# Kernel tuning notes

Measured on AMD Instinct MI355X. Metric: run time of the kernel, lower is better.

## Reference

```python
import jax, jax.numpy as jnp
import numpy as np

N, D_IN, H, L, K, Q = 131072, 384, 256, 32, 512, 4


def _lin_init(key, fan_in, fan_out):
    s = 1.0 / np.sqrt(fan_in)
    kw, kb = jax.random.split(key)
    w = jax.random.uniform(kw, (fan_in, fan_out), minval=-s, maxval=s, dtype=jnp.float32)
    b = jax.random.uniform(kb, (fan_out,), minval=-s, maxval=s, dtype=jnp.float32)
    return w, b


def setup_inputs() -> dict:
    key = jax.random.key(0)
    ks = jax.random.split(key, 8)
    enc_w1, enc_b1 = _lin_init(ks[1], D_IN, H)
    enc_w2, enc_b2 = _lin_init(ks[2], H, H)
    enc_w3, enc_b3 = _lin_init(ks[3], H, L)
    dec_w1, dec_b1 = _lin_init(ks[4], L, H)
    dec_w2, dec_b2 = _lin_init(ks[5], H, H)
    dec_w3, dec_b3 = _lin_init(ks[6], H, D_IN)
    codebooks = jax.random.normal(ks[7], (Q, K, L), dtype=jnp.float32) * 0.02
    x = jax.random.normal(ks[0], (N, D_IN), dtype=jnp.float32)
    return dict(x=x,
                enc_w1=enc_w1, enc_b1=enc_b1, enc_w2=enc_w2, enc_b2=enc_b2,
                enc_w3=enc_w3, enc_b3=enc_b3,
                dec_w1=dec_w1, dec_b1=dec_b1, dec_w2=dec_w2, dec_b2=dec_b2,
                dec_w3=dec_w3, dec_b3=dec_b3,
                codebooks=codebooks)


def _encoder(x, w1, b1, w2, b2, w3, b3):
    h = jax.nn.relu(x @ w1 + b1)
    h = jax.nn.relu(h @ w2 + b2)
    return h @ w3 + b3


def _decoder(z, w1, b1, w2, b2, w3, b3):
    h = jax.nn.relu(z @ w1 + b1)
    h = jax.nn.relu(h @ w2 + b2)
    return h @ w3 + b3


def _residual_vq(z, codebooks):
    """Residual VQ: Q stages of nearest-codeword lookup on the running residual.
    Returns (z_quantized with straight-through, indices [N,Q], commitment loss)."""
    residual = z
    quant_sum = jnp.zeros_like(z)
    indices = []
    commit = jnp.float32(0.0)
    for q in range(codebooks.shape[0]):  # small fixed loop over quantizer stages
        cb = codebooks[q]  # [K, L]
        # squared L2 distances [N, K] via expansion (cdist + argmin)
        d = (jnp.sum(residual * residual, axis=-1, keepdims=True)
             - 2.0 * residual @ cb.T
             + jnp.sum(cb * cb, axis=-1))
        idx = jnp.argmin(d, axis=-1)          # [N]
        qv = cb[idx]                          # gather [N, L]
        commit = commit + jnp.mean((jax.lax.stop_gradient(qv) - residual) ** 2)
        quant_sum = quant_sum + qv
        residual = residual - jax.lax.stop_gradient(qv)
        indices.append(idx)
    # straight-through estimator
    z_q = z + jax.lax.stop_gradient(quant_sum - z)
    return z_q, jnp.stack(indices, axis=-1), commit


def reference(x, enc_w1, enc_b1, enc_w2, enc_b2, enc_w3, enc_b3,
              dec_w1, dec_b1, dec_w2, dec_b2, dec_w3, dec_b3, codebooks):
    z = _encoder(x, enc_w1, enc_b1, enc_w2, enc_b2, enc_w3, enc_b3)
    z_q, indices, commit = _residual_vq(z, codebooks)
    x_recon = _decoder(z_q, dec_w1, dec_b1, dec_w2, dec_b2, dec_w3, dec_b3)
    return x_recon, indices, commit
```

## Files before the change

### kernel.cpp

```cpp
#include <hip/hip_runtime.h>
#include <hip/hip_bf16.h>
#include <math.h>


#define N_ROWS 131072
#define D_IN   384
#define H_DIM  256
#define L_DIM  32
#define K_CB   512
#define Q_ST   4
#define VQ_ROWS 256
#define NPART  (N_ROWS / VQ_ROWS)

typedef __attribute__((ext_vector_type(8))) short short8v;
typedef __attribute__((ext_vector_type(4))) float f32x4;

__device__ __forceinline__ ushort f2bf(float v)
{
    __hip_bfloat16 b = __float2bfloat16(v);
    return *reinterpret_cast<ushort*>(&b);
}

__device__ __forceinline__ float np_sumsq32(const float* __restrict__ v)
{
    #pragma clang fp contract(off)
    float s0 = v[0]*v[0], s1 = v[1]*v[1], s2 = v[2]*v[2], s3 = v[3]*v[3];
    float s4 = v[4]*v[4], s5 = v[5]*v[5], s6 = v[6]*v[6], s7 = v[7]*v[7];
    s0 = s0 + v[8]*v[8];   s1 = s1 + v[9]*v[9];   s2 = s2 + v[10]*v[10]; s3 = s3 + v[11]*v[11];
    s4 = s4 + v[12]*v[12]; s5 = s5 + v[13]*v[13]; s6 = s6 + v[14]*v[14]; s7 = s7 + v[15]*v[15];
    s0 = s0 + v[16]*v[16]; s1 = s1 + v[17]*v[17]; s2 = s2 + v[18]*v[18]; s3 = s3 + v[19]*v[19];
    s4 = s4 + v[20]*v[20]; s5 = s5 + v[21]*v[21]; s6 = s6 + v[22]*v[22]; s7 = s7 + v[23]*v[23];
    s0 = s0 + v[24]*v[24]; s1 = s1 + v[25]*v[25]; s2 = s2 + v[26]*v[26]; s3 = s3 + v[27]*v[27];
    s4 = s4 + v[28]*v[28]; s5 = s5 + v[29]*v[29]; s6 = s6 + v[30]*v[30]; s7 = s7 + v[31]*v[31];
    return ((s0 + s1) + (s2 + s3)) + ((s4 + s5) + (s6 + s7));
}

template<bool RELU>
__global__ __launch_bounds__(256)
void gemm_bias(const float* __restrict__ A, const float* __restrict__ B,
               const float* __restrict__ bias, float* __restrict__ C,
               int K, int Nout)
{
    #pragma clang fp contract(off)
    __shared__ float As2[32][132];
    __shared__ float Bs[32][128];
    const int t  = threadIdx.x;
    const int tc = t & 15;
    const int tr = t >> 4;
    const size_t row0 = (size_t)blockIdx.x * 128;
    const int    col0 = blockIdx.y * 128;

    float acc[8][8];
    #pragma unroll
    for (int i = 0; i < 8; ++i)
        #pragma unroll
        for (int j = 0; j < 8; ++j) acc[i][j] = 0.f;

    const int ar = t >> 3, ak = (t & 7) << 2;
    const int br = t >> 5, bc = (t & 31) << 2;

    for (int k0 = 0; k0 < K; k0 += 32) {
        #pragma unroll
        for (int i = 0; i < 4; ++i) {
            int r = ar + (i << 5);
            float4 v = *reinterpret_cast<const float4*>(A + (row0 + r) * (size_t)K + k0 + ak);
            As2[ak + 0][r] = v.x; As2[ak + 1][r] = v.y;
            As2[ak + 2][r] = v.z; As2[ak + 3][r] = v.w;
        }
        #pragma unroll
        for (int i = 0; i < 4; ++i) {
            int r = br + (i << 3);
            float4 v = *reinterpret_cast<const float4*>(B + (size_t)(k0 + r) * Nout + col0 + bc);
            *reinterpret_cast<float4*>(&Bs[r][bc]) = v;
        }
        __syncthreads();
        #pragma unroll
        for (int k = 0; k < 32; ++k) {
            float a[8], b[8];
            *reinterpret_cast<float4*>(&a[0]) = *reinterpret_cast<const float4*>(&As2[k][tr << 3]);
            *reinterpret_cast<float4*>(&a[4]) = *reinterpret_cast<const float4*>(&As2[k][(tr << 3) + 4]);
            *reinterpret_cast<float4*>(&b[0]) = *reinterpret_cast<const float4*>(&Bs[k][tc << 2]);
            *reinterpret_cast<float4*>(&b[4]) = *reinterpret_cast<const float4*>(&Bs[k][(tc << 2) + 64]);
            #pragma unroll
            for (int i = 0; i < 8; ++i)
                #pragma unroll
                for (int j = 0; j < 8; ++j) acc[i][j] = fmaf(a[i], b[j], acc[i][j]);
        }
        __syncthreads();
    }

    #pragma unroll
    for (int i = 0; i < 8; ++i) {
        size_t r = row0 + (tr << 3) + i;
        int c1 = col0 + (tc << 2);
        int c2 = c1 + 64;
        float v1[4], v2[4];
        #pragma unroll
        for (int j = 0; j < 4; ++j) {
            float u1 = acc[i][j]     + bias[c1 + j];
            float u2 = acc[i][j + 4] + bias[c2 + j];
            if (RELU) { u1 = fmaxf(u1, 0.0f); u2 = fmaxf(u2, 0.0f); }
            v1[j] = u1; v2[j] = u2;
        }
        *reinterpret_cast<float4*>(C + r * Nout + c1) = *reinterpret_cast<float4*>(&v1[0]);
        *reinterpret_cast<float4*>(C + r * Nout + c2) = *reinterpret_cast<float4*>(&v2[0]);
    }
}

__global__ __launch_bounds__(256)
void gemm_z(const float* __restrict__ A, const float* __restrict__ W,
            const float* __restrict__ bv, float* __restrict__ Z)
{
    #pragma clang fp contract(off)
    __shared__ float As2[32][132];
    __shared__ float Ws[32][36];
    const int t = threadIdx.x;
    const int cgz = t & 7, rgz = t >> 3;
    const size_t row0 = (size_t)blockIdx.x * 128;

    float acc[4][4];
    #pragma unroll
    for (int i = 0; i < 4; ++i)
        #pragma unroll
        for (int j = 0; j < 4; ++j) acc[i][j] = 0.f;

    const int ar = t >> 3, ak = (t & 7) << 2;
    for (int k0 = 0; k0 < H_DIM; k0 += 32) {
        #pragma unroll
        for (int i = 0; i < 4; ++i) {
            int r = ar + (i << 5);
            float4 v = *reinterpret_cast<const float4*>(A + (row0 + r) * (size_t)H_DIM + k0 + ak);
            As2[ak + 0][r] = v.x; As2[ak + 1][r] = v.y;
            As2[ak + 2][r] = v.z; As2[ak + 3][r] = v.w;
        }
        {
            int kr = t >> 3, cc = (t & 7) << 2;
            float4 v = *reinterpret_cast<const float4*>(W + (size_t)(k0 + kr) * L_DIM + cc);
            *reinterpret_cast<float4*>(&Ws[kr][cc]) = v;
        }
        __syncthreads();
        #pragma unroll
        for (int k = 0; k < 32; ++k) {
            float a[4], w[4];
            *reinterpret_cast<float4*>(&a[0]) = *reinterpret_cast<const float4*>(&As2[k][rgz << 2]);
            *reinterpret_cast<float4*>(&w[0]) = *reinterpret_cast<const float4*>(&Ws[k][cgz << 2]);
            #pragma unroll
            for (int i = 0; i < 4; ++i)
                #pragma unroll
                for (int j = 0; j < 4; ++j) acc[i][j] = fmaf(a[i], w[j], acc[i][j]);
        }
        __syncthreads();
    }
    #pragma unroll
    for (int i = 0; i < 4; ++i) {
        size_t row = row0 + (rgz << 2) + i;
        float v[4];
        #pragma unroll
        for (int j = 0; j < 4; ++j) v[j] = acc[i][j] + bv[(cgz << 2) + j];
        *reinterpret_cast<float4*>(Z + row * L_DIM + (cgz << 2)) = *reinterpret_cast<float4*>(&v[0]);
    }
}

__global__ __launch_bounds__(256)
void cnorm_kernel(const float* __restrict__ cbs, float* __restrict__ cnorm)
{
    #pragma clang fp contract(off)
    int g = blockIdx.x * 256 + threadIdx.x;
    const float* c = cbs + (size_t)g * L_DIM;
    float cl[L_DIM];
    #pragma unroll
    for (int l = 0; l < L_DIM; ++l) cl[l] = c[l];
    cnorm[g] = np_sumsq32(cl);
}

__global__ __launch_bounds__(256)
void prep_wt(const float* __restrict__ W, ushort* __restrict__ Wt, int K, int N)
{
    int g = blockIdx.x * 256 + threadIdx.x;
    if (g >= K * N) return;
    int n = g / K, k = g - n * K;
    Wt[g] = f2bf(W[(size_t)k * N + n]);
}

__global__ __launch_bounds__(256, 2)
void vq3_kernel(const float* __restrict__ zbuf, const float* __restrict__ cbs,
                const float* __restrict__ cnorm_g, ushort* __restrict__ zqb,
                float* __restrict__ idxOut, double* __restrict__ commitPart,
                int rowBase)
{
    #pragma clang fp contract(off)
    __shared__ float  cbL[K_CB * L_DIM];
    __shared__ float  cnL[K_CB];
    __shared__ double sred[256];

    const int t = threadIdx.x;
    const size_t lrow = (size_t)blockIdx.x * VQ_ROWS + t;
    const size_t grow = (size_t)rowBase + lrow;

    float z[L_DIM], r[L_DIM];
    {
        const float4* zp = reinterpret_cast<const float4*>(zbuf + lrow * L_DIM);
        #pragma unroll
        for (int j = 0; j < 8; ++j) {
            float4 v = zp[j];
            z[4*j+0]=v.x; z[4*j+1]=v.y; z[4*j+2]=v.z; z[4*j+3]=v.w;
        }
        #pragma unroll
        for (int l = 0; l < L_DIM; ++l) r[l] = z[l];
    }

    int bidx[Q_ST];
    double cAcc = 0.0;

    #pragma unroll 1
    for (int q = 0; q < Q_ST; ++q) {
        __syncthreads();
        {
            const float4* src = reinterpret_cast<const float4*>(cbs + (size_t)q * K_CB * L_DIM);
            float4* dst = reinterpret_cast<float4*>(cbL);
            #pragma unroll
            for (int i = 0; i < 16; ++i) dst[t + (i << 8)] = src[t + (i << 8)];
            cnL[t]       = cnorm_g[q * K_CB + t];
            cnL[t + 256] = cnorm_g[q * K_CB + t + 256];
        }
        __syncthreads();

        float rr = np_sumsq32(r);
        float bd = __builtin_inff();
        int   bi = 0;
        #pragma unroll 1
        for (int c = 0; c < K_CB; c += 2) {
            const float4* w0 = reinterpret_cast<const float4*>(cbL + (c << 5));
            const float4* w1 = w0 + 8;
            float a0 = 0.f, a1 = 0.f;
            #pragma unroll
            for (int j = 0; j < 8; ++j) {
                float4 u = w0[j], v = w1[j];
                a0 = fmaf(r[4*j+0], u.x, a0);  a1 = fmaf(r[4*j+0], v.x, a1);
                a0 = fmaf(r[4*j+1], u.y, a0);  a1 = fmaf(r[4*j+1], v.y, a1);
                a0 = fmaf(r[4*j+2], u.z, a0);  a1 = fmaf(r[4*j+2], v.z, a1);
                a0 = fmaf(r[4*j+3], u.w, a0);  a1 = fmaf(r[4*j+3], v.w, a1);
            }
            float d0 = (rr - 2.0f * a0) + cnL[c];
            float d1 = (rr - 2.0f * a1) + cnL[c + 1];
            if (d0 < bd) { bd = d0; bi = c; }
            if (d1 < bd) { bd = d1; bi = c + 1; }
        }
        bidx[q] = bi;

        {
            const float4* pw = reinterpret_cast<const float4*>(cbL + (bi << 5));
            float cs = 0.f;
            #pragma unroll
            for (int j = 0; j < 8; ++j) {
                float4 v = pw[j];
                float df;
                df = v.x - r[4*j+0]; cs = fmaf(df, df, cs); r[4*j+0] = r[4*j+0] - v.x;
                df = v.y - r[4*j+1]; cs = fmaf(df, df, cs); r[4*j+1] = r[4*j+1] - v.y;
                df = v.z - r[4*j+2]; cs = fmaf(df, df, cs); r[4*j+2] = r[4*j+2] - v.z;
                df = v.w - r[4*j+3]; cs = fmaf(df, df, cs); r[4*j+3] = r[4*j+3] - v.w;
            }
            cAcc += (double)cs;
        }
    }

    {
        float4 iv = make_float4((float)bidx[0], (float)bidx[1], (float)bidx[2], (float)bidx[3]);
        *reinterpret_cast<float4*>(idxOut + grow * Q_ST) = iv;
    }

    {
        ushort zq16[L_DIM];
        #pragma unroll
        for (int l = 0; l < L_DIM; ++l) zq16[l] = f2bf(z[l] - r[l]);
        uint4* o = reinterpret_cast<uint4*>(zqb + lrow * L_DIM);
        const uint4* s = reinterpret_cast<const uint4*>(zq16);
        #pragma unroll
        for (int j = 0; j < 4; ++j) o[j] = s[j];
    }

    sred[t] = cAcc;
    __syncthreads();
    for (int s = 128; s > 0; s >>= 1) {
        if (t < s) sred[t] += sred[t + s];
        __syncthreads();
    }
    if (t == 0) commitPart[rowBase / VQ_ROWS + blockIdx.x] = sred[0];
}

template<bool RELU, bool OUTBF16>
__global__ __launch_bounds__(256)
void mfma_gemm(const ushort* __restrict__ A, const ushort* __restrict__ Bt,
               const float* __restrict__ bias, void* __restrict__ Cout,
               int K, int Nout)
{
    __shared__ ushort As[128][40];
    __shared__ ushort Bs[128][40];
    const int t    = threadIdx.x;
    const int lane = t & 63;
    const int wid  = t >> 6;
    const int wr = wid >> 1, wc = wid & 1;
    const size_t row0 = (size_t)blockIdx.x * 128;
    const int    col0 = blockIdx.y * 128;

    f32x4 acc[4][4] = {};
    const int srow = t >> 1;
    const int sh   = (t & 1) << 4;

    for (int k0 = 0; k0 < K; k0 += 32) {
        {
            const ushort* ap = A + (row0 + srow) * (size_t)K + k0 + sh;
            uint4 v0 = *reinterpret_cast<const uint4*>(ap);
            uint4 v1 = *reinterpret_cast<const uint4*>(ap + 8);
            *reinterpret_cast<uint4*>(&As[srow][sh])     = v0;
            *reinterpret_cast<uint4*>(&As[srow][sh + 8]) = v1;
            const ushort* bp = Bt + (size_t)(col0 + srow) * K + k0 + sh;
            uint4 w0 = *reinterpret_cast<const uint4*>(bp);
            uint4 w1 = *reinterpret_cast<const uint4*>(bp + 8);
            *reinterpret_cast<uint4*>(&Bs[srow][sh])     = w0;
            *reinterpret_cast<uint4*>(&Bs[srow][sh + 8]) = w1;
        }
        __syncthreads();
        const int l15 = lane & 15, lk = (lane >> 4) << 3;
        short8v af[4], bf[4];
        #pragma unroll
        for (int f = 0; f < 4; ++f) {
            af[f] = *reinterpret_cast<const short8v*>(&As[(wr << 6) + (f << 4) + l15][lk]);
            bf[f] = *reinterpret_cast<const short8v*>(&Bs[(wc << 6) + (f << 4) + l15][lk]);
        }
        #pragma unroll
        for (int i = 0; i < 4; ++i)
            #pragma unroll
            for (int j = 0; j < 4; ++j)
                acc[i][j] = __builtin_amdgcn_mfma_f32_16x16x32_bf16(af[i], bf[j], acc[i][j], 0, 0, 0);
        __syncthreads();
    }

    const int l15 = lane & 15, lr4 = (lane >> 4) << 2;
    #pragma unroll
    for (int i = 0; i < 4; ++i) {
        #pragma unroll
        for (int j = 0; j < 4; ++j) {
            int col = col0 + (wc << 6) + (j << 4) + l15;
            float bv = bias[col];
            #pragma unroll
            for (int rj = 0; rj < 4; ++rj) {
                size_t row = row0 + (wr << 6) + (i << 4) + lr4 + rj;
                float v = acc[i][j][rj] + bv;
                if (RELU) v = fmaxf(v, 0.f);
                if (OUTBF16)
                    reinterpret_cast<ushort*>(Cout)[row * Nout + col] = f2bf(v);
                else
                    reinterpret_cast<float*>(Cout)[row * Nout + col] = v;
            }
        }
    }
}

__global__ __launch_bounds__(256)
void commit_finalize(const double* __restrict__ commitPart, float* __restrict__ outCommit)
{
    __shared__ double sred[256];
    const int t = threadIdx.x;
    double s = 0.0;
    for (int i = t; i < NPART; i += 256) s += commitPart[i];
    sred[t] = s;
    __syncthreads();
    for (int st = 128; st > 0; st >>= 1) {
        if (t < st) sred[t] += sred[t + st];
        __syncthreads();
    }
    if (t == 0)
        outCommit[0] = (float)(sred[0] / ((double)N_ROWS * (double)L_DIM));
}

extern "C" void kernel_launch(void* const* d_in, const int* in_sizes, int n_in,
                              void* d_out, int out_size, void* d_ws, size_t ws_size,
                              hipStream_t stream)
{
    const float* x      = (const float*)d_in[0];
    const float* enc_w1 = (const float*)d_in[1];
    const float* enc_b1 = (const float*)d_in[2];
    const float* enc_w2 = (const float*)d_in[3];
    const float* enc_b2 = (const float*)d_in[4];
    const float* enc_w3 = (const float*)d_in[5];
    const float* enc_b3 = (const float*)d_in[6];
    const float* dec_w1 = (const float*)d_in[7];
    const float* dec_b1 = (const float*)d_in[8];
    const float* dec_w2 = (const float*)d_in[9];
    const float* dec_b2 = (const float*)d_in[10];
    const float* dec_w3 = (const float*)d_in[11];
    const float* dec_b3 = (const float*)d_in[12];
    const float* cbs    = (const float*)d_in[13];

    float* out       = (float*)d_out;
    float* xrec      = out;
    float* idxOut    = out + (size_t)N_ROWS * D_IN;
    float* commitOut = idxOut + (size_t)N_ROWS * Q_ST;

    char*   wsb        = (char*)d_ws;
    float*  cnorm      = (float*)wsb;
    double* commitPart = (double*)(wsb + 8192);
    ushort* w1t        = (ushort*)(wsb + 12288);
    ushort* w2t        = (ushort*)(wsb + 28672);
    ushort* w3t        = (ushort*)(wsb + 159744);
    char*   bufs       = wsb + 360448;

    size_t availB = (ws_size > 360448) ? ws_size - 360448 : 0;
    long long chunk = (long long)(availB / 3264);
    chunk = (chunk / 256) * 256;
    if (chunk > N_ROWS) chunk = N_ROWS;
    if (chunk < 256) chunk = 256;

    float*  zbuf = (float*)bufs;
    float*  bufA = zbuf + (size_t)chunk * L_DIM;
    float*  bufB = bufA + (size_t)chunk * H_DIM;
    ushort* zqb  = (ushort*)(bufB + (size_t)chunk * H_DIM);
    ushort* h1b  = zqb + (size_t)chunk * L_DIM;
    ushort* h2b  = h1b + (size_t)chunk * H_DIM;

    cnorm_kernel<<<8, 256, 0, stream>>>(cbs, cnorm);
    prep_wt<<<(L_DIM  * H_DIM + 255) / 256, 256, 0, stream>>>(dec_w1, w1t, L_DIM, H_DIM);
    prep_wt<<<(H_DIM * H_DIM + 255) / 256, 256, 0, stream>>>(dec_w2, w2t, H_DIM, H_DIM);
    prep_wt<<<(H_DIM * D_IN + 255) / 256, 256, 0, stream>>>(dec_w3, w3t, H_DIM, D_IN);

    for (long long ro = 0; ro < N_ROWS; ro += chunk) {
        long long R = N_ROWS - ro;
        if (R > chunk) R = chunk;
        dim3 g2((unsigned)(R / 128), 2);
        dim3 g3((unsigned)(R / 128), 3);
        gemm_bias<true><<<g2, 256, 0, stream>>>(x + ro * D_IN, enc_w1, enc_b1, bufA, D_IN, H_DIM);
        gemm_bias<true><<<g2, 256, 0, stream>>>(bufA, enc_w2, enc_b2, bufB, H_DIM, H_DIM);
        gemm_z<<<(unsigned)(R / 128), 256, 0, stream>>>(bufB, enc_w3, enc_b3, zbuf);
        vq3_kernel<<<(unsigned)(R / VQ_ROWS), 256, 0, stream>>>(zbuf, cbs, cnorm, zqb,
                                                                idxOut, commitPart, (int)ro);
        mfma_gemm<true,  true ><<<g2, 256, 0, stream>>>(zqb, w1t, dec_b1, h1b, L_DIM, H_DIM);
        mfma_gemm<true,  true ><<<g2, 256, 0, stream>>>(h1b, w2t, dec_b2, h2b, H_DIM, H_DIM);
        mfma_gemm<false, false><<<g3, 256, 0, stream>>>(h2b, w3t, dec_b3, xrec + ro * D_IN, H_DIM, D_IN);
    }

    commit_finalize<<<1, 256, 0, stream>>>(commitPart, commitOut);
}
```

Baseline: 946.0 us.

## Split VQ codebook search across four waves per row and drop LDS staging

The VQ kernel now handles 64 rows per block, and each of the four waves scans a 128-entry slice of the codebook for the same rows. Per-wave minima are merged through shared memory, and codeword reads come straight from global memory instead of a shared-memory copy of the whole codebook. This removes the 64KB LDS footprint, raising occupancy and quadrupling the number of blocks available to fill the GPU. In exchange it adds two block syncs per stage and depends on cache-served, wave-uniform global loads. The commitPart buffer grows, so the workspace offsets move.

```diff
diff --git a/kernel.cpp b/kernel.cpp
--- a/kernel.cpp
+++ b/kernel.cpp
@@ -9,8 +9,8 @@
 #define L_DIM  32
 #define K_CB   512
 #define Q_ST   4
-#define VQ_ROWS 256
-#define NPART  (N_ROWS / VQ_ROWS)
+#define VQ_RPB 64
+#define NPART  (N_ROWS / VQ_RPB)
 
 typedef __attribute__((ext_vector_type(8))) short short8v;
 typedef __attribute__((ext_vector_type(4))) float f32x4;
@@ -182,31 +182,32 @@
     Wt[g] = f2bf(W[(size_t)k * N + n]);
 }
 
-__global__ __launch_bounds__(256, 2)
-void vq3_kernel(const float* __restrict__ zbuf, const float* __restrict__ cbs,
+__global__ __launch_bounds__(256)
+void vq6_kernel(const float* __restrict__ zbuf, const float* __restrict__ cbs,
                 const float* __restrict__ cnorm_g, ushort* __restrict__ zqb,
                 float* __restrict__ idxOut, double* __restrict__ commitPart,
                 int rowBase)
 {
     #pragma clang fp contract(off)
-    __shared__ float  cbL[K_CB * L_DIM];
-    __shared__ float  cnL[K_CB];
+    __shared__ float  sd[4][64];
+    __shared__ int    si[4][64];
     __shared__ double sred[256];
 
     const int t = threadIdx.x;
-    const size_t lrow = (size_t)blockIdx.x * VQ_ROWS + t;
+    const int w = t >> 6;
+    const int l = t & 63;
+    const size_t lrow = (size_t)blockIdx.x * VQ_RPB + l;
     const size_t grow = (size_t)rowBase + lrow;
-
-    float z[L_DIM], r[L_DIM];
+    const int c0 = w << 7;
+
+    float r[L_DIM];
     {
         const float4* zp = reinterpret_cast<const float4*>(zbuf + lrow * L_DIM);
         #pragma unroll
         for (int j = 0; j < 8; ++j) {
             float4 v = zp[j];
-            z[4*j+0]=v.x; z[4*j+1]=v.y; z[4*j+2]=v.z; z[4*j+3]=v.w;
-        }
-        #pragma unroll
-        for (int l = 0; l < L_DIM; ++l) r[l] = z[l];
+            r[4*j+0]=v.x; r[4*j+1]=v.y; r[4*j+2]=v.z; r[4*j+3]=v.w;
+        }
     }
 
     int bidx[Q_ST];
@@ -214,23 +215,17 @@
 
     #pragma unroll 1
     for (int q = 0; q < Q_ST; ++q) {
-        __syncthreads();
-        {
-            const float4* src = reinterpret_cast<const float4*>(cbs + (size_t)q * K_CB * L_DIM);
-            float4* dst = reinterpret_cast<float4*>(cbL);
-            #pragma unroll
-            for (int i = 0; i < 16; ++i) dst[t + (i << 8)] = src[t + (i << 8)];
-            cnL[t]       = cnorm_g[q * K_CB + t];
-            cnL[t + 256] = cnorm_g[q * K_CB + t + 256];
-        }
-        __syncthreads();
+        const float* cbq = cbs + (size_t)q * K_CB * L_DIM;
+        const float* cnq = cnorm_g + q * K_CB;
 
         float rr = np_sumsq32(r);
         float bd = __builtin_inff();
-        int   bi = 0;
-        #pragma unroll 1
-        for (int c = 0; c < K_CB; c += 2) {
-            const float4* w0 = reinterpret_cast<const float4*>(cbL + (c << 5));
+        int   bi = c0;
+
+        #pragma unroll 2
+        for (int cc = 0; cc < 128; cc += 2) {
+            const int c = c0 + cc;
+            const float4* w0 = reinterpret_cast<const float4*>(cbq + ((size_t)c << 5));
             const float4* w1 = w0 + 8;
             float a0 = 0.f, a1 = 0.f;
             #pragma unroll
@@ -241,15 +236,27 @@
                 a0 = fmaf(r[4*j+2], u.z, a0);  a1 = fmaf(r[4*j+2], v.z, a1);
                 a0 = fmaf(r[4*j+3], u.w, a0);  a1 = fmaf(r[4*j+3], v.w, a1);
             }
-            float d0 = (rr - 2.0f * a0) + cnL[c];
-            float d1 = (rr - 2.0f * a1) + cnL[c + 1];
+            float d0 = (rr - 2.0f * a0) + cnq[c];
+            float d1 = (rr - 2.0f * a1) + cnq[c + 1];
             if (d0 < bd) { bd = d0; bi = c; }
             if (d1 < bd) { bd = d1; bi = c + 1; }
         }
-        bidx[q] = bi;
+
+        __syncthreads();
+        sd[w][l] = bd;
+        si[w][l] = bi;
+        __syncthreads();
+
+        float gb = sd[0][l]; int gi = si[0][l];
+        #pragma unroll
+        for (int ww = 1; ww < 4; ++ww) {
+            float od = sd[ww][l]; int oi = si[ww][l];
+            if (od < gb) { gb = od; gi = oi; }
+        }
+        bidx[q] = gi;
 
         {
-            const float4* pw = reinterpret_cast<const float4*>(cbL + (bi << 5));
+            const float4* pw = reinterpret_cast<const float4*>(cbq + ((size_t)gi << 5));
             float cs = 0.f;
             #pragma unroll
             for (int j = 0; j < 8; ++j) {
@@ -264,28 +271,33 @@
         }
     }
 
-    {
+    if (w == 0) {
         float4 iv = make_float4((float)bidx[0], (float)bidx[1], (float)bidx[2], (float)bidx[3]);
         *reinterpret_cast<float4*>(idxOut + grow * Q_ST) = iv;
-    }
-
-    {
+
+        const float4* zp = reinterpret_cast<const float4*>(zbuf + lrow * L_DIM);
         ushort zq16[L_DIM];
         #pragma unroll
-        for (int l = 0; l < L_DIM; ++l) zq16[l] = f2bf(z[l] - r[l]);
+        for (int j = 0; j < 8; ++j) {
+            float4 v = zp[j];
+            zq16[4*j+0] = f2bf(v.x - r[4*j+0]);
+            zq16[4*j+1] = f2bf(v.y - r[4*j+1]);
+            zq16[4*j+2] = f2bf(v.z - r[4*j+2]);
+            zq16[4*j+3] = f2bf(v.w - r[4*j+3]);
+        }
         uint4* o = reinterpret_cast<uint4*>(zqb + lrow * L_DIM);
         const uint4* s = reinterpret_cast<const uint4*>(zq16);
         #pragma unroll
         for (int j = 0; j < 4; ++j) o[j] = s[j];
     }
 
-    sred[t] = cAcc;
+    sred[t] = (w == 0) ? cAcc : 0.0;
     __syncthreads();
     for (int s = 128; s > 0; s >>= 1) {
         if (t < s) sred[t] += sred[t + s];
         __syncthreads();
     }
-    if (t == 0) commitPart[rowBase / VQ_ROWS + blockIdx.x] = sred[0];
+    if (t == 0) commitPart[rowBase / VQ_RPB + blockIdx.x] = sred[0];
 }
 
 template<bool RELU, bool OUTBF16>
@@ -401,12 +413,12 @@
     char*   wsb        = (char*)d_ws;
     float*  cnorm      = (float*)wsb;
     double* commitPart = (double*)(wsb + 8192);
-    ushort* w1t        = (ushort*)(wsb + 12288);
-    ushort* w2t        = (ushort*)(wsb + 28672);
-    ushort* w3t        = (ushort*)(wsb + 159744);
-    char*   bufs       = wsb + 360448;
-
-    size_t availB = (ws_size > 360448) ? ws_size - 360448 : 0;
+    ushort* w1t        = (ushort*)(wsb + 24576);
+    ushort* w2t        = (ushort*)(wsb + 40960);
+    ushort* w3t        = (ushort*)(wsb + 172032);
+    char*   bufs       = wsb + 368640;
+
+    size_t availB = (ws_size > 368640) ? ws_size - 368640 : 0;
     long long chunk = (long long)(availB / 3264);
     chunk = (chunk / 256) * 256;
     if (chunk > N_ROWS) chunk = N_ROWS;
@@ -432,8 +444,8 @@
         gemm_bias<true><<<g2, 256, 0, stream>>>(x + ro * D_IN, enc_w1, enc_b1, bufA, D_IN, H_DIM);
         gemm_bias<true><<<g2, 256, 0, stream>>>(bufA, enc_w2, enc_b2, bufB, H_DIM, H_DIM);
         gemm_z<<<(unsigned)(R / 128), 256, 0, stream>>>(bufB, enc_w3, enc_b3, zbuf);
-        vq3_kernel<<<(unsigned)(R / VQ_ROWS), 256, 0, stream>>>(zbuf, cbs, cnorm, zqb,
-                                                                idxOut, commitPart, (int)ro);
+        vq6_kernel<<<(unsigned)(R / VQ_RPB), 256, 0, stream>>>(zbuf, cbs, cnorm, zqb,
+                                                               idxOut, commitPart, (int)ro);
         mfma_gemm<true,  true ><<<g2, 256, 0, stream>>>(zqb, w1t, dec_b1, h1b, L_DIM, H_DIM);
         mfma_gemm<true,  true ><<<g2, 256, 0, stream>>>(h1b, w2t, dec_b2, h2b, H_DIM, H_DIM);
         mfma_gemm<false, false><<<g3, 256, 0, stream>>>(h2b, w3t, dec_b3, xrec + ro * D_IN, H_DIM, D_IN);
```

Measured after the change: 1.586 ms. 67.6% more time.
